# Kernel optimization log

Measured on AMD Instinct MI355X. Metric: run time of the kernel, lower is better.

The kernel has to match this reference:

```python
import jax, jax.numpy as jnp
import numpy as np

# Dimensions derived from init_kwargs
NODE_NUMBER = 4096
IN_FEATURES = 2
N_KERNELS = 1
S = NODE_NUMBER * IN_FEATURES            # input_size = 8192
OUT = S * N_KERNELS                      # output size = 8192
NNZ = 524288                             # number of (row, col, weight_pos) triples
WNUM = 30000                             # shared weight pool size
BNUM = 100                               # shared bias pool size


def setup_inputs() -> dict:
    key = jax.random.key(0)
    ks = jax.random.split(key, 7)
    bound = 1.0 / np.sqrt(WNUM)  # init scale as in the torch module
    return {
        "x": jax.random.normal(ks[0], (S,), dtype=jnp.float32),
        "Param_W": (jax.random.normal(ks[1], (WNUM,), dtype=jnp.float32) * bound).astype(jnp.float32),
        "Param_b": (jax.random.normal(ks[2], (BNUM,), dtype=jnp.float32) * bound).astype(jnp.float32),
        "rows": jax.random.randint(ks[3], (NNZ,), 0, S, dtype=jnp.int32),
        "cols": jax.random.randint(ks[4], (NNZ,), 0, OUT, dtype=jnp.int32),
        "wpos": jax.random.randint(ks[5], (NNZ,), 0, WNUM, dtype=jnp.int32),
        "bias_pos": jax.random.randint(ks[6], (OUT,), 0, BNUM, dtype=jnp.int32),
    }


def reference(x, Param_W, Param_b, rows, cols, wpos, bias_pos):
    # Gather shared scalar parameters into the dense per-graph weight matrix
    # W[row, col] = Param_W[weight_pos]  (precomputed label-based index map)
    W = jnp.zeros((S, OUT), dtype=x.dtype).at[rows, cols].set(Param_W[wpos])
    # Gather per-position bias from shared bias pool (indexed by node label)
    b = Param_b[bias_pos]
    # Convolution-like matmul: flattened node features times gathered matrix
    return x @ W + b
```

## Files before the change

kernel.cpp:

```cpp
#include <hip/hip_runtime.h>

#define NNZ_ 524288
#define OUT_ 8192

__global__ void __launch_bounds__(256) fused_kernel(
    const int* __restrict__ rows, const int* __restrict__ cols,
    const int* __restrict__ wpos, const float* __restrict__ W,
    const float* __restrict__ x, const float* __restrict__ b,
    const int* __restrict__ bias_pos,
    int* __restrict__ tbl, float* __restrict__ out)
{
    const int i = blockIdx.x * 256 + threadIdx.x;
    if (i < OUT_) atomicAdd(&out[i], b[bias_pos[i]]);

    const int r = rows[i], c = cols[i];
    const int old = atomicMax(&tbl[(r << 13) | c], i);
    if (old < i) {
        float v = x[r] * W[wpos[i]];
        if (old >= 0) v -= x[rows[old]] * W[wpos[old]];
        atomicAdd(&out[c], v);
    }
}

extern "C" void kernel_launch(void* const* d_in, const int* in_sizes, int n_in,
                              void* d_out, int out_size, void* d_ws, size_t ws_size,
                              hipStream_t stream) {
    const float* x    = (const float*)d_in[0];
    const float* Pw   = (const float*)d_in[1];
    const float* Pb   = (const float*)d_in[2];
    const int*   rows = (const int*)d_in[3];
    const int*   cols = (const int*)d_in[4];
    const int*   wpos = (const int*)d_in[5];
    const int*   bpos = (const int*)d_in[6];
    float*       out  = (float*)d_out;

    int* tbl = (int*)d_ws;

    fused_kernel<<<NNZ_ / 256, 256, 0, stream>>>(
        rows, cols, wpos, Pw, x, Pb, bpos, tbl, out);
}
```

Measured before the change: 113.4 us.

## Replace dense last-writer table with bitmap duplicate detection and hash fixup

The single kernel used a 256MB dense (row,col) table with atomicMax to keep only the last writer per entry. The new code splits the work into two kernels. The first adds every contribution unconditionally and marks seen and duplicate keys in compact 8MB bitmaps. The second handles only the duplicated keys: it uses a small open-addressing hash table to find the last writer and subtracts the superseded contributions. This shrinks the random-access working set from 256MB to tens of MB, at the cost of a 16MB memset, a second launch and a hash table that depends on the workspace being pre-filled with the 0xAA pattern.

```diff
diff --git a/kernel.cpp b/kernel.cpp
--- a/kernel.cpp
+++ b/kernel.cpp
@@ -1,24 +1,62 @@
 #include <hip/hip_runtime.h>
 
-#define NNZ_ 524288
-#define OUT_ 8192
+#define NNZ_   524288
+#define OUT_   8192
+#define HSLOTS 65536
+#define HMASK  (HSLOTS - 1u)
+#define POISON 0xAAAAAAAAAAAAAAAAull
 
-__global__ void __launch_bounds__(256) fused_kernel(
+__global__ void __launch_bounds__(256) mark_add_kernel(
     const int* __restrict__ rows, const int* __restrict__ cols,
     const int* __restrict__ wpos, const float* __restrict__ W,
     const float* __restrict__ x, const float* __restrict__ b,
     const int* __restrict__ bias_pos,
-    int* __restrict__ tbl, float* __restrict__ out)
+    unsigned* __restrict__ seen, unsigned* __restrict__ dup,
+    float* __restrict__ out)
 {
     const int i = blockIdx.x * 256 + threadIdx.x;
     if (i < OUT_) atomicAdd(&out[i], b[bias_pos[i]]);
+    const int r = rows[i], c = cols[i];
+    atomicAdd(&out[c], x[r] * W[wpos[i]]);
+    const unsigned key = ((unsigned)r << 13) | (unsigned)c;
+    const unsigned w = key >> 5, bit = 1u << (key & 31u);
+    const unsigned old = atomicOr(&seen[w], bit);
+    if (old & bit) atomicOr(&dup[w], bit);
+}
 
+__global__ void __launch_bounds__(256) fix_kernel(
+    const int* __restrict__ rows, const int* __restrict__ cols,
+    const int* __restrict__ wpos, const float* __restrict__ W,
+    const float* __restrict__ x, const unsigned* __restrict__ dup,
+    unsigned long long* __restrict__ hash, float* __restrict__ out)
+{
+    const int i = blockIdx.x * 256 + threadIdx.x;
     const int r = rows[i], c = cols[i];
-    const int old = atomicMax(&tbl[(r << 13) | c], i);
-    if (old < i) {
-        float v = x[r] * W[wpos[i]];
-        if (old >= 0) v -= x[rows[old]] * W[wpos[old]];
-        atomicAdd(&out[c], v);
+    const unsigned key = ((unsigned)r << 13) | (unsigned)c;
+    if (!((dup[key >> 5] >> (key & 31u)) & 1u)) return;
+
+    const unsigned long long kh     = (unsigned long long)(key + 1u);
+    const unsigned long long packed = (kh << 19) | (unsigned)i;
+    unsigned s = (key * 2654435761u) >> 16;
+    while (true) {
+        s &= HMASK;
+        unsigned long long cur = hash[s];
+        while (cur == POISON) {
+            unsigned long long prev = atomicCAS(&hash[s], cur, packed);
+            if (prev == cur) return;
+            cur = prev;
+        }
+        if ((cur >> 19) == kh) {
+            const unsigned long long old = atomicMax(&hash[s], packed);
+            if (old < packed) {
+                const int oi = (int)(old & 0x7FFFFull);
+                atomicAdd(&out[c], -x[r] * W[wpos[oi]]);
+            } else {
+                atomicAdd(&out[c], -x[r] * W[wpos[i]]);
+            }
+            return;
+        }
+        ++s;
     }
 }
 
@@ -34,8 +72,13 @@
     const int*   bpos = (const int*)d_in[6];
     float*       out  = (float*)d_out;
 
-    int* tbl = (int*)d_ws;
+    unsigned* seen = (unsigned*)d_ws;
+    unsigned* dup  = (unsigned*)((char*)d_ws + (8u << 20));
+    unsigned long long* hash = (unsigned long long*)((char*)d_ws + (16u << 20));
 
-    fused_kernel<<<NNZ_ / 256, 256, 0, stream>>>(
-        rows, cols, wpos, Pw, x, Pb, bpos, tbl, out);
+    hipMemsetAsync(d_ws, 0, 16u << 20, stream);
+    mark_add_kernel<<<NNZ_ / 256, 256, 0, stream>>>(rows, cols, wpos, Pw, x,
+                                                    Pb, bpos, seen, dup, out);
+    fix_kernel     <<<NNZ_ / 256, 256, 0, stream>>>(rows, cols, wpos, Pw, x,
+                                                    dup, hash, out);
 }
```

After: 132.7 us. +16.9%, slower.
